# Kernel optimization log

Measured on AMD Instinct MI355X. Metric: run time of the kernel, lower is better.

## Reference

```python
import jax, jax.numpy as jnp
import numpy as np

B, S, D_IN = 2, 2048, 2048
N_HEADS, N_KV, HEAD_DIM = 16, 4, 128
GROUP = N_HEADS // N_KV  # 4
SCALING = 256.0 ** -0.5  # query_pre_attn_scalar = 256
EPS = 1e-6


def rms_norm(x, scale):
    # RMSNorm over last dim (head_dim)
    var = jnp.mean(jnp.square(x), axis=-1, keepdims=True)
    return x * jax.lax.rsqrt(var + EPS) * scale


def apply_rope(x, cos, sin):
    # x: [b, h, s, d]; cos/sin: [s, d]
    d = x.shape[-1]
    x1, x2 = x[..., : d // 2], x[..., d // 2 :]
    rotated = jnp.concatenate([-x2, x1], axis=-1)
    return x * cos[None, None, :, :] + rotated * sin[None, None, :, :]


def setup_inputs() -> dict:
    key = jax.random.key(0)
    ks = jax.random.split(key, 6)
    x = jax.random.normal(ks[0], (B, S, D_IN), dtype=jnp.float32)
    Wq = jax.random.normal(ks[1], (D_IN, N_HEADS * HEAD_DIM), dtype=jnp.float32) * 0.02
    Wk = jax.random.normal(ks[2], (D_IN, N_KV * HEAD_DIM), dtype=jnp.float32) * 0.02
    Wv = jax.random.normal(ks[3], (D_IN, N_KV * HEAD_DIM), dtype=jnp.float32) * 0.02
    Wo = jax.random.normal(ks[4], (N_HEADS * HEAD_DIM, D_IN), dtype=jnp.float32) * 0.02
    q_scale = jnp.ones((HEAD_DIM,), dtype=jnp.float32)
    k_scale = jnp.ones((HEAD_DIM,), dtype=jnp.float32)
    # RoPE tables: angles repeated twice across head_dim
    inv_freq = 1.0 / (10000.0 ** (np.arange(0, HEAD_DIM, 2, dtype=np.float32) / HEAD_DIM))
    angles = np.arange(S, dtype=np.float32)[:, None] * inv_freq[None, :]  # [S, d/2]
    angles = np.concatenate([angles, angles], axis=-1)  # [S, d]
    cos = jnp.asarray(np.cos(angles), dtype=jnp.float32)
    sin = jnp.asarray(np.sin(angles), dtype=jnp.float32)
    # causal mask: True = masked (future positions)
    mask = jnp.triu(jnp.ones((S, S), dtype=bool), k=1)
    return {"x": x, "mask": mask, "cos": cos, "sin": sin,
            "Wq": Wq, "Wk": Wk, "Wv": Wv, "Wo": Wo,
            "q_scale": q_scale, "k_scale": k_scale}


def reference(x, mask, cos, sin, Wq, Wk, Wv, Wo, q_scale, k_scale):
    b, s, _ = x.shape
    q = (x @ Wq).reshape(b, s, N_HEADS, HEAD_DIM).transpose(0, 2, 1, 3)  # [b,h,s,d]
    k = (x @ Wk).reshape(b, s, N_KV, HEAD_DIM).transpose(0, 2, 1, 3)     # [b,g,s,d]
    v = (x @ Wv).reshape(b, s, N_KV, HEAD_DIM).transpose(0, 2, 1, 3)
    # qk-norm
    q = rms_norm(q, q_scale)
    k = rms_norm(k, k_scale)
    # RoPE
    q = apply_rope(q, cos, sin)
    k = apply_rope(k, cos, sin)
    # repeat KV across groups
    k = jnp.repeat(k, GROUP, axis=1)  # [b,h,s,d]
    v = jnp.repeat(v, GROUP, axis=1)
    q = q * SCALING
    scores = jnp.einsum('bhqd,bhkd->bhqk', q, k)
    scores = jnp.where(mask, -jnp.inf, scores)
    weights = jax.nn.softmax(scores, axis=-1)
    ctx = jnp.einsum('bhqk,bhkd->bhqd', weights, v)
    ctx = ctx.transpose(0, 2, 1, 3).reshape(b, s, N_HEADS * HEAD_DIM)
    return ctx @ Wo
```

## Files before the change

### kernel.cpp

```cpp
#include <hip/hip_runtime.h>
#include <hip/hip_bf16.h>


using u16 = unsigned short;
using u32 = unsigned int;

constexpr int Ss  = 2048;
constexpr int Hh  = 16;
constexpr int KVH = 4;

typedef __attribute__((ext_vector_type(8))) short bf16x8;
typedef __attribute__((ext_vector_type(4))) float f32x4;

__device__ inline float b2f(u16 v)  { return __uint_as_float(((u32)v) << 16); }
__device__ inline u16 f2bf(float x) {
  u32 u = __float_as_uint(x);
  return (u16)((u + 0x7fffu + ((u >> 16) & 1u)) >> 16);
}
__device__ inline u32 cvtpk(float lo, float hi) {
  u32 r;
  asm("v_cvt_pk_bf16_f32 %0, %1, %2" : "=v"(r) : "v"(lo), "v"(hi));
  return r;
}

typedef const __attribute__((address_space(1))) unsigned int gas_u32;
typedef __attribute__((address_space(3))) unsigned int las_u32;
__device__ inline void gl16(const void* g, void* l) {
  __builtin_amdgcn_global_load_lds((gas_u32*)g, (las_u32*)l, 16, 0, 0);
}

__global__ __launch_bounds__(256) void cvt_bf16(const float* __restrict__ in,
                                                u16* __restrict__ out, int n4) {
  int i = blockIdx.x * 256 + threadIdx.x;
  if (i < n4) {
    float4 f = reinterpret_cast<const float4*>(in)[i];
    ushort4 o;
    o.x = f2bf(f.x); o.y = f2bf(f.y); o.z = f2bf(f.z); o.w = f2bf(f.w);
    reinterpret_cast<ushort4*>(out)[i] = o;
  }
}

__global__ __launch_bounds__(256) void tcvt(const float* __restrict__ in,
                                            u16* __restrict__ out, int N, int K) {
  __shared__ u16 T[64][66];
  const int k0 = blockIdx.x * 64, n0 = blockIdx.y * 64;
  const int c = threadIdx.x & 63, rb = threadIdx.x >> 6;
#pragma unroll
  for (int p = 0; p < 16; p++) {
    int r = p * 4 + rb;
    T[c][r] = f2bf(in[(size_t)(k0 + r) * N + n0 + c]);
  }
  __syncthreads();
#pragma unroll
  for (int p = 0; p < 16; p++) {
    int nr = p * 4 + rb;
    out[(size_t)(n0 + nr) * K + k0 + c] = T[nr][c];
  }
}

__global__ __launch_bounds__(256) void vtrans(const u16* __restrict__ kv,
                                              u16* __restrict__ vT) {
  __shared__ u16 T[64][66];
  const int s0 = blockIdx.x * 64, d0 = blockIdx.y * 64, z = blockIdx.z;
  const int b = z >> 2, kvh = z & 3;
  const int c = threadIdx.x & 63, rb = threadIdx.x >> 6;
#pragma unroll
  for (int p = 0; p < 16; p++) {
    int r = p * 4 + rb;
    T[c][r] = kv[(size_t)(b * Ss + s0 + r) * 1024 + 512 + kvh * 128 + d0 + c];
  }
  __syncthreads();
#pragma unroll
  for (int p = 0; p < 16; p++) {
    int dr = p * 4 + rb;
    vT[((size_t)z * 128 + d0 + dr) * Ss + s0 + c] = T[dr][c];
  }
}

template <int OUT_F32>
__global__ __launch_bounds__(256) void gemm_bt(const u16* __restrict__ A,
                                               const u16* __restrict__ Bt,
                                               void* __restrict__ C,
                                               int N, int K) {
  __shared__ u16 As[128 * 64];
  __shared__ u16 Bs[128 * 64];
  const int t = threadIdx.x, w = t >> 6, lane = t & 63;
  const int lrow = lane & 15, quad = lane >> 4;
  const int wm = w & 1, wn = w >> 1;
  const int m0 = blockIdx.x * 128, n0 = blockIdx.y * 128;

  f32x4 acc[4][4];
#pragma unroll
  for (int i = 0; i < 4; i++)
#pragma unroll
    for (int j = 0; j < 4; j++) acc[i][j] = (f32x4)0.f;

  const int srow = t >> 3;
  const int scol = (t & 7) * 8;

  for (int k0 = 0; k0 < K; k0 += 64) {
#pragma unroll
    for (int c = 0; c < 4; c++) {
      gl16(A + (size_t)(m0 + c * 32 + srow) * K + k0 + scol,
           (char*)As + c * 4096 + t * 16);
      gl16(Bt + (size_t)(n0 + c * 32 + srow) * K + k0 + scol,
           (char*)Bs + c * 4096 + t * 16);
    }
    __syncthreads();
#pragma unroll
    for (int kc = 0; kc < 2; kc++) {
      bf16x8 af[4], bfr[4];
#pragma unroll
      for (int i = 0; i < 4; i++) {
        af[i] = *reinterpret_cast<const bf16x8*>(
            &As[(wm * 64 + i * 16 + lrow) * 64 + kc * 32 + quad * 8]);
        bfr[i] = *reinterpret_cast<const bf16x8*>(
            &Bs[(wn * 64 + i * 16 + lrow) * 64 + kc * 32 + quad * 8]);
      }
#pragma unroll
      for (int mi = 0; mi < 4; mi++)
#pragma unroll
        for (int ni = 0; ni < 4; ni++)
          acc[mi][ni] =
              __builtin_amdgcn_mfma_f32_16x16x32_bf16(af[mi], bfr[ni], acc[mi][ni], 0, 0, 0);
    }
    __syncthreads();
  }

#pragma unroll
  for (int mi = 0; mi < 4; mi++)
#pragma unroll
    for (int ni = 0; ni < 4; ni++)
#pragma unroll
      for (int r = 0; r < 4; r++) {
        int row = m0 + wm * 64 + mi * 16 + quad * 4 + r;
        int col = n0 + wn * 64 + ni * 16 + lrow;
        if (OUT_F32)
          reinterpret_cast<float*>(C)[(size_t)row * N + col] = acc[mi][ni][r];
        else
          reinterpret_cast<u16*>(C)[(size_t)row * N + col] = f2bf(acc[mi][ni][r]);
      }
}

__global__ __launch_bounds__(256) void rmsrope2(u16* __restrict__ qbuf,
                                                u16* __restrict__ kvb,
                                                const float* __restrict__ qsc,
                                                const float* __restrict__ ksc,
                                                const float* __restrict__ cosb,
                                                const float* __restrict__ sinb) {
  const int w = threadIdx.x >> 6, lane = threadIdx.x & 63;
  const int vi = blockIdx.x * 4 + w;
  const int tok = vi / 20, j = vi - tok * 20;
  const int s = tok & (Ss - 1);
  const bool isq = j < 16;
  u16* p = isq ? (qbuf + (size_t)tok * 2048 + j * 128)
               : (kvb + (size_t)tok * 1024 + (j - 16) * 128);
  const float* scale = isq ? qsc : ksc;
  const float mult = isq ? 0.0625f : 1.0f;
  float e0 = b2f(p[lane]), e1 = b2f(p[lane + 64]);
  float ss = e0 * e0 + e1 * e1;
#pragma unroll
  for (int off = 32; off > 0; off >>= 1) ss += __shfl_xor(ss, off);
  float rr = rsqrtf(ss * (1.0f / 128.0f) + 1e-6f);
  float x0 = e0 * rr * scale[lane];
  float x1 = e1 * rr * scale[lane + 64];
  float c0 = cosb[s * 128 + lane], c1 = cosb[s * 128 + 64 + lane];
  float sn0 = sinb[s * 128 + lane], sn1 = sinb[s * 128 + 64 + lane];
  p[lane]      = f2bf((x0 * c0 - x1 * sn0) * mult);
  p[lane + 64] = f2bf((x1 * c1 + x0 * sn1) * mult);
}

__global__ __launch_bounds__(128, 2) void attn_mfma(const u16* __restrict__ qb,
                                                    const u16* __restrict__ kv,
                                                    const u16* __restrict__ vT,
                                                    u16* __restrict__ ctx) {
  __shared__ u16 Ks[64 * 128];
  __shared__ u16 Vs[128 * 64];
  __shared__ u16 Ps[2][32 * 40];
  const int i = blockIdx.x;
  const int kq = i >> 8, jj = i & 255, x = jj >> 5, hb = jj & 31;
  const int qtile = (kq == 0) ? 31 - x : (kq == 1) ? x : (kq == 2) ? 23 - x : 8 + x;
  const int h = hb & 15, b = hb >> 4;
  const int t = threadIdx.x, w = t >> 6, lane = t & 63;
  const int lrow = lane & 15, quad = lane >> 4;
  const int kvh = h >> 2;
  const int qw = qtile * 64 + w * 32;

  const u16* kbase = kv + (size_t)b * Ss * 1024 + kvh * 128;
  const u16* vbase = vT + (size_t)(b * KVH + kvh) * 128 * Ss;

  const int kr  = t >> 4;
  const int kco = ((t & 15) ^ (kr & 7)) * 8;
  const int vr  = t >> 3;
  const int vco = ((t & 7) ^ (vr & 7)) * 8;
  const int sw8 = (lrow & 7) << 3;

  bf16x8 qf[2][4];
#pragma unroll
  for (int g = 0; g < 2; g++)
#pragma unroll
    for (int c = 0; c < 4; c++)
      qf[g][c] = *reinterpret_cast<const bf16x8*>(
          qb + ((size_t)(b * Ss + qw + g * 16 + lrow) * Hh + h) * 128 + c * 32 + quad * 8);

  f32x4 o[2][8];
#pragma unroll
  for (int g = 0; g < 2; g++)
#pragma unroll
    for (int n = 0; n < 8; n++) o[g][n] = (f32x4)0.f;
  float mx[2] = {-1e30f, -1e30f}, ls[2] = {0.f, 0.f};

  const int ntile = qtile + 1;
  for (int kt = 0; kt < ntile; kt++) {
    const int kb0 = kt * 64;
    __syncthreads();
#pragma unroll
    for (int p8 = 0; p8 < 8; p8++) {
      gl16(kbase + (size_t)(kb0 + p8 * 8 + kr) * 1024 + kco,
           (char*)Ks + (p8 * 128 + t) * 16);
      gl16(vbase + (size_t)(p8 * 16 + vr) * Ss + kb0 + vco,
           (char*)Vs + (p8 * 128 + t) * 16);
    }
    __syncthreads();

    f32x4 st[2][4];
#pragma unroll
    for (int g = 0; g < 2; g++)
#pragma unroll
      for (int mt = 0; mt < 4; mt++) st[g][mt] = (f32x4)0.f;
#pragma unroll
    for (int c = 0; c < 4; c++) {
      bf16x8 kf[4];
#pragma unroll
      for (int mt = 0; mt < 4; mt++)
        kf[mt] = *reinterpret_cast<const bf16x8*>(
            &Ks[(mt * 16 + lrow) * 128 + ((((c * 4 + quad) << 3)) ^ sw8)]);
      __builtin_amdgcn_s_setprio(1);
#pragma unroll
      for (int mt = 0; mt < 4; mt++)
#pragma unroll
        for (int g = 0; g < 2; g++)
          st[g][mt] =
              __builtin_amdgcn_mfma_f32_16x16x32_bf16(kf[mt], qf[g][c], st[g][mt], 0, 0, 0);
      __builtin_amdgcn_s_setprio(0);
    }
    if (kb0 + 63 > qw) {
#pragma unroll
      for (int g = 0; g < 2; g++) {
        int qg = qw + g * 16 + lrow;
#pragma unroll
        for (int mt = 0; mt < 4; mt++) {
          int kg = kb0 + mt * 16 + quad * 4;
#pragma unroll
          for (int r = 0; r < 4; r++)
            st[g][mt][r] = (kg + r > qg) ? -1e30f : st[g][mt][r];
        }
      }
    }
    float tmv[2];
#pragma unroll
    for (int g = 0; g < 2; g++) {
      f32x4 m4;
#pragma unroll
      for (int r = 0; r < 4; r++)
        m4[r] = fmaxf(fmaxf(st[g][0][r], st[g][1][r]), fmaxf(st[g][2][r], st[g][3][r]));
      float tm = fmaxf(fmaxf(m4[0], m4[1]), fmaxf(m4[2], m4[3]));
      tm = fmaxf(tm, __shfl_xor(tm, 16));
      tm = fmaxf(tm, __shfl_xor(tm, 32));
      tmv[g] = tm;
    }
    if (__any((tmv[0] > mx[0] + 8.0f) || (tmv[1] > mx[1] + 8.0f))) {
#pragma unroll
      for (int g = 0; g < 2; g++) {
        float mn = fmaxf(mx[g], tmv[g]);
        float a = __expf(mx[g] - mn);
        mx[g] = mn;
        ls[g] *= a;
#pragma unroll
        for (int n = 0; n < 8; n++) o[g][n] *= a;
      }
    }
#pragma unroll
    for (int g = 0; g < 2; g++) {
      float tsum = 0.f;
#pragma unroll
      for (int mt = 0; mt < 4; mt++)
#pragma unroll
        for (int r = 0; r < 4; r++) {
          float pv = __expf(st[g][mt][r] - mx[g]);
          st[g][mt][r] = pv;
          tsum += pv;
        }
      tsum += __shfl_xor(tsum, 16);
      tsum += __shfl_xor(tsum, 32);
      ls[g] += tsum;
    }
#pragma unroll
    for (int c2 = 0; c2 < 2; c2++) {
#pragma unroll
      for (int g = 0; g < 2; g++)
#pragma unroll
        for (int mh = 0; mh < 2; mh++) {
          const f32x4 sv = st[g][c2 * 2 + mh];
          uint2 pk;
          pk.x = cvtpk(sv[0], sv[1]);
          pk.y = cvtpk(sv[2], sv[3]);
          *reinterpret_cast<uint2*>(
              &Ps[w][(g * 16 + lrow) * 40 + mh * 16 + quad * 4]) = pk;
        }
      bf16x8 pfr[2];
#pragma unroll
      for (int g = 0; g < 2; g++)
        pfr[g] = *reinterpret_cast<const bf16x8*>(
            &Ps[w][(g * 16 + lrow) * 40 + quad * 8]);
      __builtin_amdgcn_s_setprio(1);
#pragma unroll
      for (int n = 0; n < 8; n++) {
        bf16x8 vf = *reinterpret_cast<const bf16x8*>(
            &Vs[(n * 16 + lrow) * 64 + ((((c2 * 4 + quad) << 3)) ^ sw8)]);
#pragma unroll
        for (int g = 0; g < 2; g++)
          o[g][n] = __builtin_amdgcn_mfma_f32_16x16x32_bf16(vf, pfr[g], o[g][n], 0, 0, 0);
      }
      __builtin_amdgcn_s_setprio(0);
    }
  }

#pragma unroll
  for (int g = 0; g < 2; g++) {
    float linv = 1.0f / ls[g];
    u16* obase = ctx + ((size_t)(b * Ss + qw + g * 16 + lrow) * Hh + h) * 128 + quad * 4;
#pragma unroll
    for (int n = 0; n < 8; n++) {
      uint2 pk;
      pk.x = cvtpk(o[g][n][0] * linv, o[g][n][1] * linv);
      pk.y = cvtpk(o[g][n][2] * linv, o[g][n][3] * linv);
      *reinterpret_cast<uint2*>(obase + n * 16) = pk;
    }
  }
}

extern "C" void kernel_launch(void* const* d_in, const int* in_sizes, int n_in,
                              void* d_out, int out_size, void* d_ws, size_t ws_size,
                              hipStream_t stream) {
  const float* x    = (const float*)d_in[0];
  const float* cosb = (const float*)d_in[2];
  const float* sinb = (const float*)d_in[3];
  const float* Wq   = (const float*)d_in[4];
  const float* Wk   = (const float*)d_in[5];
  const float* Wv   = (const float*)d_in[6];
  const float* Wo   = (const float*)d_in[7];
  const float* qsc  = (const float*)d_in[8];
  const float* ksc  = (const float*)d_in[9];

  const int M = 2 * Ss;
  u16* xb   = (u16*)d_ws;
  u16* ctxb = xb;
  u16* Wt   = xb + (size_t)8388608;
  u16* qbuf = Wt + (size_t)4194304;
  u16* kvb  = qbuf + (size_t)8388608;
  u16* vTb  = kvb + (size_t)4194304;

  cvt_bf16<<<8192, 256, 0, stream>>>(x, xb, 2097152);

  tcvt<<<dim3(32, 32), 256, 0, stream>>>(Wq, Wt, 2048, 2048);
  gemm_bt<0><<<dim3(32, 16), 256, 0, stream>>>(xb, Wt, qbuf, 2048, 2048);

  tcvt<<<dim3(32, 8), 256, 0, stream>>>(Wk, Wt, 512, 2048);
  tcvt<<<dim3(32, 8), 256, 0, stream>>>(Wv, Wt + (size_t)512 * 2048, 512, 2048);
  gemm_bt<0><<<dim3(32, 8), 256, 0, stream>>>(xb, Wt, kvb, 1024, 2048);

  rmsrope2<<<(M * 20) / 4, 256, 0, stream>>>(qbuf, kvb, qsc, ksc, cosb, sinb);

  vtrans<<<dim3(32, 2, 8), 256, 0, stream>>>(kvb, vTb);

  attn_mfma<<<dim3(1024), 128, 0, stream>>>(qbuf, kvb, vTb, ctxb);

  tcvt<<<dim3(32, 32), 256, 0, stream>>>(Wo, Wt, 2048, 2048);
  gemm_bt<1><<<dim3(32, 16), 256, 0, stream>>>(ctxb, Wt, d_out, 2048, 2048);
}
```

Baseline: 382.3 us.

## Replace GEMM with double-buffered swizzled 256x256 tile kernel and fuse QKV projection

The 128x128 bf16 GEMM is replaced by a 512-thread kernel with 256x256 output tiles, double-buffered LDS staging, XOR-swizzled LDS columns and raised wave priority around the MFMA bursts. Q, K and V weights are transposed into one contiguous buffer, so a single launch computes all three projections and routes output columns to the q and kv buffers. Workspace is re-aliased so attention writes its context back into the q buffer. The larger tiles cut global reloads and LDS bank conflicts, and the prefetch hides load latency. In exchange, the grids shrink to 192 and 128 blocks, which leaves many CUs idle on a 256-CU part, and the in-place context write relies on each attention block only reading its own q rows.

```diff
diff --git a/kernel.cpp b/kernel.cpp
--- a/kernel.cpp
+++ b/kernel.cpp
@@ -77,69 +77,115 @@
   }
 }
 
-template <int OUT_F32>
-__global__ __launch_bounds__(256) void gemm_bt(const u16* __restrict__ A,
-                                               const u16* __restrict__ Bt,
-                                               void* __restrict__ C,
-                                               int N, int K) {
-  __shared__ u16 As[128 * 64];
-  __shared__ u16 Bs[128 * 64];
-  const int t = threadIdx.x, w = t >> 6, lane = t & 63;
+template <int MODE>
+__global__ __launch_bounds__(512, 2) void gemm256(const u16* __restrict__ A,
+                                                  const u16* __restrict__ Bt,
+                                                  void* __restrict__ C0,
+                                                  u16* __restrict__ C1,
+                                                  int K) {
+  __shared__ u16 As[2][256 * 64];
+  __shared__ u16 Bs[2][256 * 64];
+  const int t = threadIdx.x;
+  const int wid = t >> 6, lane = t & 63;
   const int lrow = lane & 15, quad = lane >> 4;
-  const int wm = w & 1, wn = w >> 1;
-  const int m0 = blockIdx.x * 128, n0 = blockIdx.y * 128;
-
-  f32x4 acc[4][4];
+  const int wm = wid >> 1, wn = wid & 1;
+  const int m0 = blockIdx.x * 256, n0 = blockIdx.y * 256;
+  const int sw8 = (lrow & 7) << 3;
+
+  const int srow = t >> 3;
+  const int sco  = ((t & 7) ^ (srow & 7)) * 8;
+
+  f32x4 acc[4][8];
 #pragma unroll
   for (int i = 0; i < 4; i++)
 #pragma unroll
-    for (int j = 0; j < 4; j++) acc[i][j] = (f32x4)0.f;
-
-  const int srow = t >> 3;
-  const int scol = (t & 7) * 8;
-
-  for (int k0 = 0; k0 < K; k0 += 64) {
-#pragma unroll
-    for (int c = 0; c < 4; c++) {
-      gl16(A + (size_t)(m0 + c * 32 + srow) * K + k0 + scol,
-           (char*)As + c * 4096 + t * 16);
-      gl16(Bt + (size_t)(n0 + c * 32 + srow) * K + k0 + scol,
-           (char*)Bs + c * 4096 + t * 16);
-    }
-    __syncthreads();
+    for (int j = 0; j < 8; j++) acc[i][j] = (f32x4)0.f;
+
+#define STAGE(buf, k0)                                                     \
+  {                                                                        \
+    _Pragma("unroll") for (int p = 0; p < 4; p++) {                        \
+      gl16(A + (size_t)(m0 + p * 64 + srow) * K + (k0) + sco,              \
+           (char*)As[buf] + (p * 512 + t) * 16);                           \
+      gl16(Bt + (size_t)(n0 + p * 64 + srow) * K + (k0) + sco,             \
+           (char*)Bs[buf] + (p * 512 + t) * 16);                           \
+    }                                                                      \
+  }
+
+  const int nk = K >> 6;
+  STAGE(0, 0)
+  STAGE(1, 64)
+  asm volatile("s_waitcnt vmcnt(8)" ::: "memory");
+  __builtin_amdgcn_s_barrier();
+  __builtin_amdgcn_sched_barrier(0);
+
+  for (int kt = 0; kt < nk; ++kt) {
+    const int buf = kt & 1;
 #pragma unroll
     for (int kc = 0; kc < 2; kc++) {
-      bf16x8 af[4], bfr[4];
-#pragma unroll
-      for (int i = 0; i < 4; i++) {
+      bf16x8 af[4], bfr[8];
+#pragma unroll
+      for (int i = 0; i < 4; i++)
         af[i] = *reinterpret_cast<const bf16x8*>(
-            &As[(wm * 64 + i * 16 + lrow) * 64 + kc * 32 + quad * 8]);
-        bfr[i] = *reinterpret_cast<const bf16x8*>(
-            &Bs[(wn * 64 + i * 16 + lrow) * 64 + kc * 32 + quad * 8]);
+            &As[buf][(wm * 64 + i * 16 + lrow) * 64 + (((kc * 4 + quad) << 3) ^ sw8)]);
+#pragma unroll
+      for (int j = 0; j < 8; j++)
+        bfr[j] = *reinterpret_cast<const bf16x8*>(
+            &Bs[buf][(wn * 128 + j * 16 + lrow) * 64 + (((kc * 4 + quad) << 3) ^ sw8)]);
+      __builtin_amdgcn_s_setprio(1);
+#pragma unroll
+      for (int i = 0; i < 4; i++)
+#pragma unroll
+        for (int j = 0; j < 8; j++)
+          acc[i][j] =
+              __builtin_amdgcn_mfma_f32_16x16x32_bf16(af[i], bfr[j], acc[i][j], 0, 0, 0);
+      __builtin_amdgcn_s_setprio(0);
+    }
+    __builtin_amdgcn_sched_barrier(0);
+    __builtin_amdgcn_s_barrier();
+    __builtin_amdgcn_sched_barrier(0);
+    if (kt + 2 < nk) {
+      STAGE(buf, (kt + 2) * 64)
+    }
+    if (kt + 1 < nk) {
+      if (kt + 2 < nk) {
+        asm volatile("s_waitcnt vmcnt(8)" ::: "memory");
+      } else {
+        asm volatile("s_waitcnt vmcnt(0)" ::: "memory");
       }
-#pragma unroll
-      for (int mi = 0; mi < 4; mi++)
-#pragma unroll
-        for (int ni = 0; ni < 4; ni++)
-          acc[mi][ni] =
-              __builtin_amdgcn_mfma_f32_16x16x32_bf16(af[mi], bfr[ni], acc[mi][ni], 0, 0, 0);
-    }
-    __syncthreads();
-  }
-
-#pragma unroll
-  for (int mi = 0; mi < 4; mi++)
-#pragma unroll
-    for (int ni = 0; ni < 4; ni++)
-#pragma unroll
-      for (int r = 0; r < 4; r++) {
-        int row = m0 + wm * 64 + mi * 16 + quad * 4 + r;
-        int col = n0 + wn * 64 + ni * 16 + lrow;
-        if (OUT_F32)
-          reinterpret_cast<float*>(C)[(size_t)row * N + col] = acc[mi][ni][r];
-        else
-          reinterpret_cast<u16*>(C)[(size_t)row * N + col] = f2bf(acc[mi][ni][r]);
-      }
+      __builtin_amdgcn_s_barrier();
+      __builtin_amdgcn_sched_barrier(0);
+    }
+  }
+#undef STAGE
+
+  if (MODE == 0) {
+    u16* C;
+    int stride, coff;
+    if (n0 < 2048) { C = (u16*)C0; stride = 2048; coff = n0; }
+    else           { C = C1;       stride = 1024; coff = n0 - 2048; }
+#pragma unroll
+    for (int i = 0; i < 4; i++)
+#pragma unroll
+      for (int j = 0; j < 8; j++)
+#pragma unroll
+        for (int r = 0; r < 4; r++) {
+          int row = m0 + wm * 64 + i * 16 + quad * 4 + r;
+          int col = coff + wn * 128 + j * 16 + lrow;
+          C[(size_t)row * stride + col] = f2bf(acc[i][j][r]);
+        }
+  } else {
+    float* C = (float*)C0;
+#pragma unroll
+    for (int i = 0; i < 4; i++)
+#pragma unroll
+      for (int j = 0; j < 8; j++)
+#pragma unroll
+        for (int r = 0; r < 4; r++) {
+          int row = m0 + wm * 64 + i * 16 + quad * 4 + r;
+          int col = n0 + wn * 128 + j * 16 + lrow;
+          C[(size_t)row * 2048 + col] = acc[i][j][r];
+        }
+  }
 }
 
 __global__ __launch_bounds__(256) void rmsrope2(u16* __restrict__ qbuf,
@@ -355,27 +401,26 @@
 
   const int M = 2 * Ss;
   u16* xb   = (u16*)d_ws;
-  u16* ctxb = xb;
-  u16* Wt   = xb + (size_t)8388608;
-  u16* qbuf = Wt + (size_t)4194304;
+  u16* Wqkv = xb + (size_t)8388608;
+  u16* qbuf = Wqkv + (size_t)6291456;
   u16* kvb  = qbuf + (size_t)8388608;
-  u16* vTb  = kvb + (size_t)4194304;
+  u16* vTb  = xb;
+  u16* WoT  = Wqkv;
 
   cvt_bf16<<<8192, 256, 0, stream>>>(x, xb, 2097152);
 
-  tcvt<<<dim3(32, 32), 256, 0, stream>>>(Wq, Wt, 2048, 2048);
-  gemm_bt<0><<<dim3(32, 16), 256, 0, stream>>>(xb, Wt, qbuf, 2048, 2048);
-
-  tcvt<<<dim3(32, 8), 256, 0, stream>>>(Wk, Wt, 512, 2048);
-  tcvt<<<dim3(32, 8), 256, 0, stream>>>(Wv, Wt + (size_t)512 * 2048, 512, 2048);
-  gemm_bt<0><<<dim3(32, 8), 256, 0, stream>>>(xb, Wt, kvb, 1024, 2048);
+  tcvt<<<dim3(32, 32), 256, 0, stream>>>(Wq, Wqkv, 2048, 2048);
+  tcvt<<<dim3(32, 8), 256, 0, stream>>>(Wk, Wqkv + (size_t)2048 * 2048, 512, 2048);
+  tcvt<<<dim3(32, 8), 256, 0, stream>>>(Wv, Wqkv + (size_t)2560 * 2048, 512, 2048);
+
+  gemm256<0><<<dim3(16, 12), 512, 0, stream>>>(xb, Wqkv, qbuf, kvb, 2048);
 
   rmsrope2<<<(M * 20) / 4, 256, 0, stream>>>(qbuf, kvb, qsc, ksc, cosb, sinb);
 
   vtrans<<<dim3(32, 2, 8), 256, 0, stream>>>(kvb, vTb);
 
-  attn_mfma<<<dim3(1024), 128, 0, stream>>>(qbuf, kvb, vTb, ctxb);
-
-  tcvt<<<dim3(32, 32), 256, 0, stream>>>(Wo, Wt, 2048, 2048);
-  gemm_bt<1><<<dim3(32, 16), 256, 0, stream>>>(ctxb, Wt, d_out, 2048, 2048);
-}
+  attn_mfma<<<dim3(1024), 128, 0, stream>>>(qbuf, kvb, vTb, qbuf );
+
+  tcvt<<<dim3(32, 32), 256, 0, stream>>>(Wo, WoT, 2048, 2048);
+  gemm256<1><<<dim3(16, 8), 512, 0, stream>>>(qbuf, WoT, d_out, nullptr, 2048);
+}
```

New measurement: 362.4 us. 5.2% less time.
